# Kernel optimization log

Hardware: AMD Instinct MI355X
Metric: run time of the kernel (lower is better)

The kernel has to match this reference:

```python
import jax, jax.numpy as jnp
import numpy as np
import math

DIM = 1024
N_HEADS = 16
HEAD_DIM = DIM // N_HEADS
BS, SEQ, NNB = 8, 1024, 50
LN_EPS = 1e-12


def setup_inputs() -> dict:
    key = jax.random.key(0)
    ks = jax.random.split(key, 12)
    std = 0.02
    inp = {
        "x": jax.random.normal(ks[0], (BS, SEQ, DIM), jnp.float32),
        "x_neighbor": jax.random.normal(ks[1], (BS, NNB, DIM), jnp.float32),
        "mask": jnp.ones((BS, SEQ), jnp.int32),
        "neighbor_mask": jnp.ones((BS, NNB), jnp.float32),
        "qw": std * jax.random.normal(ks[2], (DIM, DIM), jnp.float32),
        "qb": jnp.zeros((DIM,), jnp.float32),
        "kw": std * jax.random.normal(ks[3], (DIM, DIM), jnp.float32),
        "kb": jnp.zeros((DIM,), jnp.float32),
        "vw": std * jax.random.normal(ks[4], (DIM, DIM), jnp.float32),
        "vb": jnp.zeros((DIM,), jnp.float32),
        "ow": std * jax.random.normal(ks[5], (DIM, DIM), jnp.float32),
        "ob": jnp.zeros((DIM,), jnp.float32),
        "ln_g": jnp.ones((DIM,), jnp.float32),
        "ln_b": jnp.zeros((DIM,), jnp.float32),
    }
    return inp


def _split_heads(t, bs):
    # [bs, s, dim] -> [bs, h, s, dh]
    return t.reshape(bs, -1, N_HEADS, HEAD_DIM).transpose(0, 2, 1, 3)


def reference(x, x_neighbor, mask, neighbor_mask, qw, qb, kw, kb, vw, vb, ow, ob, ln_g, ln_b):
    bs, seq, dim = x.shape
    # mean-pool neighbors with mask
    nm = neighbor_mask[..., None]                      # [bs, nnb, 1]
    xn = (x_neighbor * nm).sum(axis=1) / nm.sum(axis=1)  # [bs, dim]
    query = jnp.broadcast_to(xn[:, None, :], x.shape)    # [bs, seq, dim]

    q = _split_heads(query @ qw.T + qb, bs) / math.sqrt(HEAD_DIM)
    k = _split_heads(x @ kw.T + kb, bs)
    v = _split_heads(x @ vw.T + vb, bs)

    scores = jnp.einsum("bhqd,bhkd->bhqk", q, k)       # [bs, h, seq, seq]
    key_mask = (mask == 0)[:, None, None, :]            # [bs, 1, 1, seq]
    scores = jnp.where(key_mask, -jnp.inf, scores)
    weights = jax.nn.softmax(scores, axis=-1)           # dropout p=0.0 -> no-op
    context = jnp.einsum("bhqk,bhkd->bhqd", weights, v)
    context = context.transpose(0, 2, 1, 3).reshape(bs, seq, dim)
    out = context @ ow.T + ob

    h = out + x
    mu = h.mean(axis=-1, keepdims=True)
    var = ((h - mu) ** 2).mean(axis=-1, keepdims=True)
    return (h - mu) / jnp.sqrt(var + LN_EPS) * ln_g + ln_b
```

## Files before the change

kernel.cpp:

```cpp
#include <hip/hip_runtime.h>
#include <hip/hip_bf16.h>


#define DIM  1024
#define NH   16
#define HD   64
#define BS   8
#define SEQ  1024
#define NNB  50

#define OF_P     16
#define OF_E     131088
#define OF_DENP  262160
#define OF_XW    266256
#define OF_CTX   397328
#define OF_OUTR  405520

__global__ void k_prep(const float* __restrict__ xnb, const float* __restrict__ nm,
                       const float* __restrict__ qw, const float* __restrict__ qb,
                       const float* __restrict__ kw, float* __restrict__ p){
  int h = blockIdx.x & 15, b = blockIdx.x >> 4;
  int tid = threadIdx.x, wv = tid >> 6, ln = tid & 63;
  __shared__ float xnl[1024];
  __shared__ float qp[256];
  __shared__ float ql[64];
  {
    int d = tid*4;
    float4 acc = {0,0,0,0}; float wsum = 0.f;
    #pragma unroll 10
    for (int n=0; n<NNB; n++){
      float w = nm[b*NNB + n];
      float4 v = *(const float4*)(xnb + (size_t)(b*NNB + n)*DIM + d);
      acc.x += w*v.x; acc.y += w*v.y; acc.z += w*v.z; acc.w += w*v.w;
      wsum += w;
    }
    float inv = 1.f/wsum;
    acc.x*=inv; acc.y*=inv; acc.z*=inv; acc.w*=inv;
    *(float4*)(xnl + d) = acc;
  }
  __syncthreads();
  {
    const float* qrow = qw + (size_t)(h*HD + ln)*DIM + wv*256;
    const float* xrow = xnl + wv*256;
    float part = 0.f;
    #pragma unroll 16
    for (int i=0; i<64; i++){
      float4 a = *(const float4*)(qrow + i*4);
      float4 c = *(const float4*)(xrow + i*4);
      part += a.x*c.x + a.y*c.y + a.z*c.z + a.w*c.w;
    }
    qp[wv*64 + ln] = part;
  }
  __syncthreads();
  if (wv == 0){
    float qv = qp[ln] + qp[64+ln] + qp[128+ln] + qp[192+ln];
    ql[ln] = (qv + qb[h*HD + ln]) * 0.125f;
  }
  __syncthreads();
  {
    int d = tid*4;
    float4 acc = {0,0,0,0};
    #pragma unroll 8
    for (int j=0; j<HD; j++){
      float qj = ql[j];
      float4 kv = *(const float4*)(kw + (size_t)(h*HD + j)*DIM + d);
      acc.x += qj*kv.x; acc.y += qj*kv.y; acc.z += qj*kv.z; acc.w += qj*kv.w;
    }
    *(float4*)(p + (size_t)(b*NH + h)*DIM + d) = acc;
  }
}

__global__ __launch_bounds__(1024, 4)
void k_swp(const float* __restrict__ x, const float* __restrict__ p,
           const int* __restrict__ mask,
           float* __restrict__ e, float* __restrict__ denp){
  int b = blockIdx.x, sc = blockIdx.y;
  int s0 = sc * 32;
  int tid = threadIdx.x, wv = tid >> 6, ln = tid & 63;
  __shared__ float wf[32*20];

  int hg = wv & 3, sq = wv >> 2;
  float acc[8][4];
  #pragma unroll
  for (int i=0; i<8; i++){ acc[i][0]=0.f; acc[i][1]=0.f; acc[i][2]=0.f; acc[i][3]=0.f; }

  #pragma unroll 1
  for (int kc=0; kc<4; kc++){
    int d = kc*256 + ln*4;
    const float* pb = p + (size_t)(b*NH + hg*4)*DIM + d;
    float4 pr0 = *(const float4*)(pb);
    float4 pr1 = *(const float4*)(pb +   (size_t)DIM);
    float4 pr2 = *(const float4*)(pb + 2*(size_t)DIM);
    float4 pr3 = *(const float4*)(pb + 3*(size_t)DIM);
    const float* xb = x + (size_t)(b*SEQ + s0 + sq*8)*DIM + d;
    #pragma unroll
    for (int sb=0; sb<8; sb+=4){
      float4 xr[4];
      #pragma unroll
      for (int u=0; u<4; u++)
        xr[u] = *(const float4*)(xb + (size_t)(sb+u)*DIM);
      #pragma unroll
      for (int u=0; u<4; u++){
        acc[sb+u][0] += xr[u].x*pr0.x + xr[u].y*pr0.y + xr[u].z*pr0.z + xr[u].w*pr0.w;
        acc[sb+u][1] += xr[u].x*pr1.x + xr[u].y*pr1.y + xr[u].z*pr1.z + xr[u].w*pr1.w;
        acc[sb+u][2] += xr[u].x*pr2.x + xr[u].y*pr2.y + xr[u].z*pr2.z + xr[u].w*pr2.w;
        acc[sb+u][3] += xr[u].x*pr3.x + xr[u].y*pr3.y + xr[u].z*pr3.z + xr[u].w*pr3.w;
      }
    }
  }
  #pragma unroll
  for (int off=1; off<64; off<<=1){
    #pragma unroll
    for (int si=0; si<8; si++){
      acc[si][0] += __shfl_xor(acc[si][0], off, 64);
      acc[si][1] += __shfl_xor(acc[si][1], off, 64);
      acc[si][2] += __shfl_xor(acc[si][2], off, 64);
      acc[si][3] += __shfl_xor(acc[si][3], off, 64);
    }
  }
  if (ln == 0){
    #pragma unroll
    for (int si=0; si<8; si++){
      float4 v; v.x = acc[si][0]; v.y = acc[si][1]; v.z = acc[si][2]; v.w = acc[si][3];
      *(float4*)(wf + (sq*8 + si)*20 + hg*4) = v;
    }
  }
  __syncthreads();
  if (tid < 512){
    int s = tid >> 4, h = tid & 15;
    float sv = wf[s*20 + h];
    float ev = mask[b*SEQ + s0 + s] ? __expf(sv) : 0.f;
    wf[s*20 + h] = ev;
    e[(size_t)(b*SEQ + s0)*NH + tid] = ev;
  }
  __syncthreads();
  if (tid < 16){
    float dsum = 0.f;
    #pragma unroll
    for (int ss=0; ss<32; ss++) dsum += wf[ss*20 + tid];
    denp[(sc*BS + b)*NH + tid] = dsum;
  }
}

__global__ __launch_bounds__(1024, 4)
void k_pool(const float* __restrict__ x, const float* __restrict__ e,
            const float* __restrict__ denp, float* __restrict__ xw){
  int b = blockIdx.x, dc = blockIdx.y;
  int tid = threadIdx.x, wv = tid >> 6, ln = tid & 63;
  int hg = wv & 3, sq = wv >> 2;
  __shared__ float elds[SEQ*NH];
  __shared__ float invd[NH];
  const float* eb = e + (size_t)b*SEQ*NH;
  #pragma unroll
  for (int it=0; it<4; it++){
    int idx = it*4096 + tid*4;
    *(float4*)(elds + idx) = *(const float4*)(eb + idx);
  }
  if (tid < NH){
    float dsum = 0.f;
    #pragma unroll
    for (int sc=0; sc<32; sc++) dsum += denp[(sc*BS + b)*NH + tid];
    invd[tid] = 1.f/dsum;
  }
  __syncthreads();
  int d = dc*256 + ln*4;
  const float* xb = x + (size_t)(b*SEQ + sq*256)*DIM + d;
  float4 a0={0,0,0,0}, a1={0,0,0,0}, a2={0,0,0,0}, a3={0,0,0,0};
  #pragma unroll 1
  for (int ss=0; ss<256; ss+=8){
    float4 xq[8];
    #pragma unroll
    for (int u=0; u<8; u++)
      xq[u] = *(const float4*)(xb + (size_t)(ss+u)*DIM);
    #pragma unroll
    for (int u=0; u<8; u++){
      float4 w = *(const float4*)(elds + (sq*256 + ss + u)*NH + hg*4);
      a0.x += xq[u].x*w.x; a0.y += xq[u].y*w.x; a0.z += xq[u].z*w.x; a0.w += xq[u].w*w.x;
      a1.x += xq[u].x*w.y; a1.y += xq[u].y*w.y; a1.z += xq[u].z*w.y; a1.w += xq[u].w*w.y;
      a2.x += xq[u].x*w.z; a2.y += xq[u].y*w.z; a2.z += xq[u].z*w.z; a2.w += xq[u].w*w.z;
      a3.x += xq[u].x*w.w; a3.y += xq[u].y*w.w; a3.z += xq[u].z*w.w; a3.w += xq[u].w*w.w;
    }
  }
  __syncthreads();
  float4* red = (float4*)elds;
  red[0*1024 + wv*64 + ln] = a0;
  red[1*1024 + wv*64 + ln] = a1;
  red[2*1024 + wv*64 + ln] = a2;
  red[3*1024 + wv*64 + ln] = a3;
  __syncthreads();
  if (sq == 0){
    #pragma unroll
    for (int q=0; q<4; q++){
      float4 s = red[q*1024 + (0*4+hg)*64 + ln];
      #pragma unroll
      for (int s4=1; s4<4; s4++){
        float4 t = red[q*1024 + (s4*4+hg)*64 + ln];
        s.x += t.x; s.y += t.y; s.z += t.z; s.w += t.w;
      }
      float iv = invd[hg*4 + q];
      s.x *= iv; s.y *= iv; s.z *= iv; s.w *= iv;
      *(float4*)(xw + (size_t)(b*NH + hg*4 + q)*DIM + d) = s;
    }
  }
}

__global__ void k_ctx(const float* __restrict__ xw, const float* __restrict__ vw,
                      const float* __restrict__ vb, float* __restrict__ ctx){
  int wv = threadIdx.x >> 6, ln = threadIdx.x & 63;
  int jo = blockIdx.x*4 + wv;
  int h  = jo >> 6;
  float acc[BS] = {0,0,0,0,0,0,0,0};
  #pragma unroll
  for (int i=0; i<4; i++){
    int d = ln*4 + 256*i;
    float4 vv = *(const float4*)(vw + (size_t)jo*DIM + d);
    #pragma unroll
    for (int b=0; b<BS; b++){
      float4 xv = *(const float4*)(xw + (size_t)(b*NH + h)*DIM + d);
      acc[b] += vv.x*xv.x + vv.y*xv.y + vv.z*xv.z + vv.w*xv.w;
    }
  }
  #pragma unroll
  for (int off=32; off>=1; off>>=1){
    #pragma unroll
    for (int b=0; b<BS; b++) acc[b] += __shfl_down(acc[b], off, 64);
  }
  if (ln == 0){
    float bias = vb[jo];
    #pragma unroll
    for (int b=0; b<BS; b++) ctx[b*DIM + jo] = acc[b] + bias;
  }
}

__global__ void k_outrow(const float* __restrict__ ctx, const float* __restrict__ ow,
                         const float* __restrict__ ob, float* __restrict__ outr){
  int wv = threadIdx.x >> 6, ln = threadIdx.x & 63;
  int io = blockIdx.x*4 + wv;
  float acc[BS] = {0,0,0,0,0,0,0,0};
  #pragma unroll
  for (int i=0; i<4; i++){
    int d = ln*4 + 256*i;
    float4 wt = *(const float4*)(ow + (size_t)io*DIM + d);
    #pragma unroll
    for (int b=0; b<BS; b++){
      float4 cv = *(const float4*)(ctx + b*DIM + d);
      acc[b] += wt.x*cv.x + wt.y*cv.y + wt.z*cv.z + wt.w*cv.w;
    }
  }
  #pragma unroll
  for (int off=32; off>=1; off>>=1){
    #pragma unroll
    for (int b=0; b<BS; b++) acc[b] += __shfl_down(acc[b], off, 64);
  }
  if (ln == 0){
    float bias = ob[io];
    #pragma unroll
    for (int b=0; b<BS; b++) outr[b*DIM + io] = acc[b] + bias;
  }
}

__global__ void k_ln(const float* __restrict__ x, const float* __restrict__ outr,
                     const float* __restrict__ g, const float* __restrict__ bt,
                     float* __restrict__ out){
  int row = blockIdx.x;
  int b = row >> 10;
  size_t base = (size_t)row * DIM;
  int tid = threadIdx.x;
  float4 xv = ((const float4*)(x + base))[tid];
  float4 ov = ((const float4*)(outr + (size_t)b*DIM))[tid];
  float4 h;
  h.x = xv.x + ov.x; h.y = xv.y + ov.y; h.z = xv.z + ov.z; h.w = xv.w + ov.w;
  float s  = h.x + h.y + h.z + h.w;
  float s2 = h.x*h.x + h.y*h.y + h.z*h.z + h.w*h.w;
  #pragma unroll
  for (int off=32; off>=1; off>>=1){
    s  += __shfl_xor(s,  off, 64);
    s2 += __shfl_xor(s2, off, 64);
  }
  __shared__ float r1[4], r2[4];
  int wv = tid >> 6, ln = tid & 63;
  if (ln == 0){ r1[wv] = s; r2[wv] = s2; }
  __syncthreads();
  s  = r1[0] + r1[1] + r1[2] + r1[3];
  s2 = r2[0] + r2[1] + r2[2] + r2[3];
  float mu   = s  * (1.f/1024.f);
  float var  = s2 * (1.f/1024.f) - mu*mu;
  float rstd = rsqrtf(var + 1e-12f);
  float4 gv = ((const float4*)g)[tid];
  float4 bv = ((const float4*)bt)[tid];
  float4 y;
  y.x = (h.x - mu)*rstd*gv.x + bv.x;
  y.y = (h.y - mu)*rstd*gv.y + bv.y;
  y.z = (h.z - mu)*rstd*gv.z + bv.z;
  y.w = (h.w - mu)*rstd*gv.w + bv.w;
  ((float4*)(out + base))[tid] = y;
}

extern "C" void kernel_launch(void* const* d_in, const int* in_sizes, int n_in,
                              void* d_out, int out_size, void* d_ws, size_t ws_size,
                              hipStream_t stream) {
  const float* x    = (const float*)d_in[0];
  const float* xnb  = (const float*)d_in[1];
  const int*   mask = (const int*  )d_in[2];
  const float* nm   = (const float*)d_in[3];
  const float* qw   = (const float*)d_in[4];
  const float* qb   = (const float*)d_in[5];
  const float* kw   = (const float*)d_in[6];
  const float* vw   = (const float*)d_in[8];
  const float* vb   = (const float*)d_in[9];
  const float* ow   = (const float*)d_in[10];
  const float* ob   = (const float*)d_in[11];
  const float* lng  = (const float*)d_in[12];
  const float* lnb  = (const float*)d_in[13];
  float* out = (float*)d_out;

  float* ws   = (float*)d_ws;
  float* p    = ws + OF_P;
  float* e    = ws + OF_E;
  float* denp = ws + OF_DENP;
  float* xw   = ws + OF_XW;
  float* ctx  = ws + OF_CTX;
  float* outr = ws + OF_OUTR;

  k_prep  <<<128,             256,  0, stream>>>(xnb, nm, qw, qb, kw, p);
  k_swp   <<<dim3(BS,32),     1024, 0, stream>>>(x, p, mask, e, denp);
  k_pool  <<<dim3(BS,4),      1024, 0, stream>>>(x, e, denp, xw);
  k_ctx   <<<256,             256,  0, stream>>>(xw, vw, vb, ctx);
  k_outrow<<<256,             256,  0, stream>>>(ctx, ow, ob, outr);
  k_ln    <<<BS*SEQ,          256,  0, stream>>>(x, outr, lng, lnb, out);
}
```

Baseline: 198.5 us.

## Split pool kernel across more column blocks with intra-wave sequence reduction

The weighted-pooling kernel now launches 16 column chunks per batch instead of 4, giving 128 blocks rather than 32. Each wave covers 64 columns, and four lane groups each stride over a quarter of the sequence rows. Partial sums are combined with cross-lane shuffles before the shared-memory reduction across waves. This aims to fill more compute units on a kernel that was too small to occupy the GPU. The cost is reloading the exp-weight array into shared memory four times as often per batch and extra shuffle work.

```diff
diff --git a/kernel.cpp b/kernel.cpp
--- a/kernel.cpp
+++ b/kernel.cpp
@@ -147,7 +147,7 @@
             const float* __restrict__ denp, float* __restrict__ xw){
   int b = blockIdx.x, dc = blockIdx.y;
   int tid = threadIdx.x, wv = tid >> 6, ln = tid & 63;
-  int hg = wv & 3, sq = wv >> 2;
+  int hg = wv & 3, rq = wv >> 2;
   __shared__ float elds[SEQ*NH];
   __shared__ float invd[NH];
   const float* eb = e + (size_t)b*SEQ*NH;
@@ -163,38 +163,54 @@
     invd[tid] = 1.f/dsum;
   }
   __syncthreads();
-  int d = dc*256 + ln*4;
-  const float* xb = x + (size_t)(b*SEQ + sq*256)*DIM + d;
+  int rs = ln >> 4;
+  int d  = dc*64 + (ln & 15)*4;
   float4 a0={0,0,0,0}, a1={0,0,0,0}, a2={0,0,0,0}, a3={0,0,0,0};
+  int sbase = rq*256 + rs;
+  const float* xb = x + (size_t)(b*SEQ + sbase)*DIM + d;
+  const float* el = elds + (size_t)sbase*NH + hg*4;
   #pragma unroll 1
-  for (int ss=0; ss<256; ss+=8){
-    float4 xq[8];
-    #pragma unroll
-    for (int u=0; u<8; u++)
-      xq[u] = *(const float4*)(xb + (size_t)(ss+u)*DIM);
-    #pragma unroll
-    for (int u=0; u<8; u++){
-      float4 w = *(const float4*)(elds + (sq*256 + ss + u)*NH + hg*4);
+  for (int it=0; it<64; it+=4){
+    float4 xq[4];
+    #pragma unroll
+    for (int u=0; u<4; u++)
+      xq[u] = *(const float4*)(xb + (size_t)(it+u)*4*DIM);
+    #pragma unroll
+    for (int u=0; u<4; u++){
+      float4 w = *(const float4*)(el + (size_t)(it+u)*4*NH);
       a0.x += xq[u].x*w.x; a0.y += xq[u].y*w.x; a0.z += xq[u].z*w.x; a0.w += xq[u].w*w.x;
       a1.x += xq[u].x*w.y; a1.y += xq[u].y*w.y; a1.z += xq[u].z*w.y; a1.w += xq[u].w*w.y;
       a2.x += xq[u].x*w.z; a2.y += xq[u].y*w.z; a2.z += xq[u].z*w.z; a2.w += xq[u].w*w.z;
       a3.x += xq[u].x*w.w; a3.y += xq[u].y*w.w; a3.z += xq[u].z*w.w; a3.w += xq[u].w*w.w;
     }
   }
+  #pragma unroll
+  for (int off=16; off<=32; off<<=1){
+    a0.x += __shfl_xor(a0.x, off, 64); a0.y += __shfl_xor(a0.y, off, 64);
+    a0.z += __shfl_xor(a0.z, off, 64); a0.w += __shfl_xor(a0.w, off, 64);
+    a1.x += __shfl_xor(a1.x, off, 64); a1.y += __shfl_xor(a1.y, off, 64);
+    a1.z += __shfl_xor(a1.z, off, 64); a1.w += __shfl_xor(a1.w, off, 64);
+    a2.x += __shfl_xor(a2.x, off, 64); a2.y += __shfl_xor(a2.y, off, 64);
+    a2.z += __shfl_xor(a2.z, off, 64); a2.w += __shfl_xor(a2.w, off, 64);
+    a3.x += __shfl_xor(a3.x, off, 64); a3.y += __shfl_xor(a3.y, off, 64);
+    a3.z += __shfl_xor(a3.z, off, 64); a3.w += __shfl_xor(a3.w, off, 64);
+  }
   __syncthreads();
   float4* red = (float4*)elds;
-  red[0*1024 + wv*64 + ln] = a0;
-  red[1*1024 + wv*64 + ln] = a1;
-  red[2*1024 + wv*64 + ln] = a2;
-  red[3*1024 + wv*64 + ln] = a3;
-  __syncthreads();
-  if (sq == 0){
+  if (ln < 16){
+    red[0*1024 + wv*16 + ln] = a0;
+    red[1*1024 + wv*16 + ln] = a1;
+    red[2*1024 + wv*16 + ln] = a2;
+    red[3*1024 + wv*16 + ln] = a3;
+  }
+  __syncthreads();
+  if (rq == 0 && ln < 16){
     #pragma unroll
     for (int q=0; q<4; q++){
-      float4 s = red[q*1024 + (0*4+hg)*64 + ln];
+      float4 s = red[q*1024 + (0*4 + hg)*16 + ln];
       #pragma unroll
-      for (int s4=1; s4<4; s4++){
-        float4 t = red[q*1024 + (s4*4+hg)*64 + ln];
+      for (int r=1; r<4; r++){
+        float4 t = red[q*1024 + (r*4 + hg)*16 + ln];
         s.x += t.x; s.y += t.y; s.z += t.z; s.w += t.w;
       }
       float iv = invd[hg*4 + q];
@@ -324,7 +340,7 @@
 
   k_prep  <<<128,             256,  0, stream>>>(xnb, nm, qw, qb, kw, p);
   k_swp   <<<dim3(BS,32),     1024, 0, stream>>>(x, p, mask, e, denp);
-  k_pool  <<<dim3(BS,4),      1024, 0, stream>>>(x, e, denp, xw);
+  k_pool  <<<dim3(BS,16),     1024, 0, stream>>>(x, e, denp, xw);
   k_ctx   <<<256,             256,  0, stream>>>(xw, vw, vb, ctx);
   k_outrow<<<256,             256,  0, stream>>>(ctx, ow, ob, outr);
   k_ln    <<<BS*SEQ,          256,  0, stream>>>(x, outr, lng, lnb, out);
```

Measured after the change: 178.6 us. 10.0% less time.
